# Optimization experiments

Hardware: AMD Instinct MI355X
Metric: run time of the kernel (lower is better)

## Reference

```python
import jax, jax.numpy as jnp
import numpy as np

IN_F = 1024
OUT_F = 4096
BATCH = 1024

def setup_inputs() -> dict:
    key = jax.random.key(0)
    k1, k2, k3, k4 = jax.random.split(key, 4)
    s = np.sqrt(IN_F).astype(np.float32)  # weight init range, as in reset_parameters
    x = jax.random.normal(k1, (BATCH, IN_F), dtype=jnp.float32)
    weights = jax.random.uniform(k2, (OUT_F, IN_F), minval=-s, maxval=s, dtype=jnp.float32)
    centers = 0.1 * jax.random.normal(k3, (OUT_F, IN_F), dtype=jnp.float32)
    # sigmas ~ U(in-0.5, in+0.5); inv_covar = 1/sigmas
    sigmas = jax.random.uniform(k4, (OUT_F, IN_F), minval=IN_F - 0.5, maxval=IN_F + 0.5, dtype=jnp.float32)
    inv_covar = 1.0 / sigmas
    return {"x": x, "weights": weights, "centers": centers, "inv_covar": inv_covar}

def reference(x, weights, centers, inv_covar):
    # linear part with FGN bias: b_i = -sum_j W_ij * C_ij
    biases = -jnp.sum(weights * centers, axis=-1)  # (O,)
    l = x @ weights.T + biases                      # (B, O)
    # diag Mahalanobis: g_bi = sum_j (x_bj - c_ij)^2 * ic_ij^2
    # expanded to GEMMs to avoid the (B, O, I) broadcast intermediate
    ic2 = inv_covar * inv_covar                     # (O, I)
    g = ((x * x) @ ic2.T
         - 2.0 * (x @ (centers * ic2).T)
         + jnp.sum(centers * centers * ic2, axis=-1))  # (B, O)
    return l * jnp.exp(-g)
```

## Files before the change

### kernel.cpp

```cpp
#include <hip/hip_runtime.h>
#include <hip/hip_bf16.h>
#include <stdint.h>


typedef __attribute__((ext_vector_type(8))) __bf16 bf16x8;
typedef __attribute__((ext_vector_type(16))) float f32x16;

#define G_SCALE 8388608.0f
#define G_INV   1.1920929e-7f

__device__ __forceinline__ unsigned short f2bf(float f) {
  union { float f; unsigned int u; } v; v.f = f;
  unsigned int u = v.u;
  return (unsigned short)((u + 0x7FFFu + ((u >> 16) & 1u)) >> 16);
}

__device__ __forceinline__ unsigned int f2f8(float f) {
  union { float f; unsigned int u; } v; v.f = f;
  unsigned int u = v.u;
  unsigned int s = (u >> 31) << 7;
  unsigned int e = (u >> 23) & 255u;
  if (e < 121u) return s;
  unsigned int q = ((e - 120u) << 23) | (u & 0x7FFFFFu);
  unsigned int r = (q + 0x7FFFFu + ((q >> 20) & 1u)) >> 20;
  if (r > 126u) r = 126u;
  return s | r;
}

__device__ __forceinline__ unsigned long long pack8f8(const float* x) {
  unsigned long long r = 0;
#pragma unroll
  for (int j = 0; j < 8; ++j) r |= (unsigned long long)f2f8(x[j]) << (8 * j);
  return r;
}

__global__ __launch_bounds__(256) void prep(
    const float* __restrict__ X, const float* __restrict__ W,
    const float* __restrict__ C, const float* __restrict__ IC,
    unsigned short* __restrict__ Wb, char* __restrict__ GBb,
    unsigned short* __restrict__ Xb, char* __restrict__ XQb,
    float* __restrict__ bias, float* __restrict__ dvec) {
  const int b = blockIdx.x;
  const int lane = threadIdx.x & 63;
  if (b < 1024) {
    const int row = b * 4 + (threadIdx.x >> 6);
    const float4* W4 = (const float4*)W + (size_t)row * 256 + lane * 4;
    const float4* C4 = (const float4*)C + (size_t)row * 256 + lane * 4;
    const float4* I4 = (const float4*)IC + (size_t)row * 256 + lane * 4;
    float wv[16], cv[16], i2[16], m2[16], i2s[16];
    float swc = 0.f, sd = 0.f;
#pragma unroll
    for (int p = 0; p < 4; ++p) {
      float4 w = W4[p], c = C4[p], ic = I4[p];
      wv[4*p] = w.x; wv[4*p+1] = w.y; wv[4*p+2] = w.z; wv[4*p+3] = w.w;
      cv[4*p] = c.x; cv[4*p+1] = c.y; cv[4*p+2] = c.z; cv[4*p+3] = c.w;
      i2[4*p] = ic.x*ic.x; i2[4*p+1] = ic.y*ic.y; i2[4*p+2] = ic.z*ic.z; i2[4*p+3] = ic.w*ic.w;
    }
#pragma unroll
    for (int j = 0; j < 16; ++j) {
      swc += wv[j] * cv[j];
      sd  += cv[j] * cv[j] * i2[j];
      i2s[j] = i2[j] * G_SCALE;
      m2[j]  = -2.f * cv[j] * i2[j] * G_SCALE;
    }
    ushort4* Wo = (ushort4*)Wb + (size_t)row * 256 + lane * 4;
#pragma unroll
    for (int p = 0; p < 4; ++p) {
      ushort4 a;
      a.x = f2bf(wv[4*p]); a.y = f2bf(wv[4*p+1]);
      a.z = f2bf(wv[4*p+2]); a.w = f2bf(wv[4*p+3]);
      Wo[p] = a;
    }
    ulonglong2* gb = (ulonglong2*)(GBb + (size_t)row * 2048 + lane * 32);
    ulonglong2 u0, u1;
    u0.x = pack8f8(i2s);     u0.y = pack8f8(m2);
    u1.x = pack8f8(i2s + 8); u1.y = pack8f8(m2 + 8);
    gb[0] = u0; gb[1] = u1;
#pragma unroll
    for (int off = 32; off > 0; off >>= 1) {
      swc += __shfl_down(swc, off);
      sd  += __shfl_down(sd, off);
    }
    if (lane == 0) { bias[row] = -swc; dvec[row] = sd; }
  } else {
    const int row = (b - 1024) * 4 + (threadIdx.x >> 6);
    const float4* X4 = (const float4*)X + (size_t)row * 256 + lane * 4;
    float xv[16], qv[16];
#pragma unroll
    for (int p = 0; p < 4; ++p) {
      float4 x = X4[p];
      xv[4*p] = x.x; xv[4*p+1] = x.y; xv[4*p+2] = x.z; xv[4*p+3] = x.w;
    }
#pragma unroll
    for (int j = 0; j < 16; ++j) qv[j] = xv[j] * xv[j];
    ushort4* Xo = (ushort4*)Xb + (size_t)row * 256 + lane * 4;
#pragma unroll
    for (int p = 0; p < 4; ++p) {
      ushort4 a;
      a.x = f2bf(xv[4*p]); a.y = f2bf(xv[4*p+1]);
      a.z = f2bf(xv[4*p+2]); a.w = f2bf(xv[4*p+3]);
      Xo[p] = a;
    }
    ulonglong2* xq = (ulonglong2*)(XQb + (size_t)row * 2048 + lane * 32);
    ulonglong2 u0, u1;
    u0.x = pack8f8(qv);     u0.y = pack8f8(xv);
    u1.x = pack8f8(qv + 8); u1.y = pack8f8(xv + 8);
    xq[0] = u0; xq[1] = u1;
  }
}

#define GLD16(gp, lp)                                                          \
  __builtin_amdgcn_global_load_lds(                                            \
      (const __attribute__((address_space(1))) unsigned int*)(gp),             \
      (__attribute__((address_space(3))) unsigned int*)(lp), 16, 0, 0)

__global__ __launch_bounds__(256, 2) void fgn_gemm(
    const char* __restrict__ Xb, const char* __restrict__ XQb,
    const char* __restrict__ Wb, const char* __restrict__ GBb,
    const float* __restrict__ bias, const float* __restrict__ dvec,
    float* __restrict__ out) {
  __shared__ char smem[73728];
  const int t = threadIdx.x;
  const int m0 = blockIdx.y * 128;
  const int n0 = blockIdx.x * 64;

  const int srow = t >> 2;
  const int gof = ((t & 3) ^ ((srow >> 1) & 3)) * 16;
  const char* gX  = Xb  + (size_t)(m0 + srow) * 2048 + gof;
  const char* gXQ = XQb + (size_t)(m0 + srow) * 2048 + gof;
  const char* gW  = Wb  + (size_t)(n0 + srow) * 2048 + gof;
  const char* gGB = GBb + (size_t)(n0 + srow) * 2048 + gof;

#define LBASE(B) (smem + (size_t)(B) * 24576)
#define STAGE(B, S)                                                            \
  do {                                                                         \
    const int ko = (S) * 64;                                                   \
    char* lb = LBASE(B);                                                       \
    GLD16(gX + ko,           lb + t * 16);                                     \
    GLD16(gX + ko + 131072,  lb + 4096 + t * 16);                              \
    GLD16(gXQ + ko,          lb + 8192 + t * 16);                              \
    GLD16(gXQ + ko + 131072, lb + 12288 + t * 16);                             \
    GLD16(gW + ko,           lb + 16384 + t * 16);                             \
    GLD16(gGB + ko,          lb + 20480 + t * 16);                             \
  } while (0)

  const int wave = t >> 6, lane = t & 63;
  const int wy = wave >> 1, wx = wave & 1;
  const int ln = lane & 31, kh = lane >> 5;
  const int sw = (ln >> 1) & 3;

  int arow[2];
#pragma unroll
  for (int mt = 0; mt < 2; ++mt) arow[mt] = (wy * 64 + mt * 32 + ln) * 64;
  const int brow = (wx * 32 + ln) * 64;

  f32x16 accL[2], accG[2];
#pragma unroll
  for (int mt = 0; mt < 2; ++mt) { accL[mt] = (f32x16)0.f; accG[mt] = (f32x16)0.f; }

#define COMPUTE(B)                                                             \
  do {                                                                         \
    char* lb = LBASE(B);                                                       \
    _Pragma("unroll")                                                          \
    for (int ks = 0; ks < 2; ++ks) {                                           \
      const int u16 = ((2 * ks + kh) ^ sw) * 16;                               \
      bf16x8 ax0 = *(const bf16x8*)(lb + arow[0] + u16);                       \
      bf16x8 ax1 = *(const bf16x8*)(lb + arow[1] + u16);                       \
      long2 xq0 = *(const long2*)(lb + 8192 + arow[0] + u16);                  \
      long2 xq1 = *(const long2*)(lb + 8192 + arow[1] + u16);                  \
      bf16x8 bw = *(const bf16x8*)(lb + 16384 + brow + u16);                   \
      long2 gb  = *(const long2*)(lb + 20480 + brow + u16);                    \
      accL[0] = __builtin_amdgcn_mfma_f32_32x32x16_bf16(ax0, bw, accL[0], 0, 0, 0); \
      accL[1] = __builtin_amdgcn_mfma_f32_32x32x16_bf16(ax1, bw, accL[1], 0, 0, 0); \
      accG[0] = __builtin_amdgcn_mfma_f32_32x32x16_fp8_fp8(xq0.x, gb.x, accG[0], 0, 0, 0); \
      accG[1] = __builtin_amdgcn_mfma_f32_32x32x16_fp8_fp8(xq1.x, gb.x, accG[1], 0, 0, 0); \
      accG[0] = __builtin_amdgcn_mfma_f32_32x32x16_fp8_fp8(xq0.y, gb.y, accG[0], 0, 0, 0); \
      accG[1] = __builtin_amdgcn_mfma_f32_32x32x16_fp8_fp8(xq1.y, gb.y, accG[1], 0, 0, 0); \
    }                                                                          \
  } while (0)

  STAGE(0, 0);
  STAGE(1, 1);
#pragma unroll 1
  for (int s = 0; s < 31; ++s) {
    __builtin_amdgcn_s_waitcnt(0x0076);
    __builtin_amdgcn_s_barrier();
    COMPUTE(s % 3);
    if (s < 30) STAGE((s + 2) % 3, s + 2);
  }
  __builtin_amdgcn_s_waitcnt(0x0070);
  __builtin_amdgcn_s_barrier();
  COMPUTE(31 % 3);

  const int col = n0 + wx * 32 + ln;
  const float bn = bias[col], dn = dvec[col];
#pragma unroll
  for (int mt = 0; mt < 2; ++mt) {
    const int rb = m0 + wy * 64 + mt * 32 + 4 * kh;
#pragma unroll
    for (int r = 0; r < 16; ++r) {
      const int row = rb + (r & 3) + 8 * (r >> 2);
      const float l = accL[mt][r] + bn;
      const float g = accG[mt][r] * G_INV + dn;
      out[(size_t)row * 4096 + col] = l * __expf(-g);
    }
  }
#undef STAGE
#undef COMPUTE
#undef LBASE
}

extern "C" void kernel_launch(void* const* d_in, const int* in_sizes, int n_in,
                              void* d_out, int out_size, void* d_ws, size_t ws_size,
                              hipStream_t stream) {
  const float* x  = (const float*)d_in[0];
  const float* W  = (const float*)d_in[1];
  const float* C  = (const float*)d_in[2];
  const float* IC = (const float*)d_in[3];
  float* out = (float*)d_out;

  char* ws = (char*)d_ws;
  unsigned short* Wb  = (unsigned short*)(ws);
  char*           GBb = ws + (8u << 20);
  unsigned short* Xb  = (unsigned short*)(ws + (16u << 20));
  char*           XQb = ws + (18u << 20);
  float* bias = (float*)(ws + (20u << 20));
  float* dvec = (float*)(ws + (20u << 20) + 16384);

  hipLaunchKernelGGL(prep, dim3(1280), dim3(256), 0, stream, x, W, C, IC,
                     Wb, GBb, Xb, XQb, bias, dvec);
  hipLaunchKernelGGL(fgn_gemm, dim3(64, 8), dim3(256), 0, stream,
                     Xb ? (const char*)Xb : nullptr, XQb,
                     (const char*)Wb, GBb, bias, dvec, out);
}
```

Before: 128.5 us.

## Pre-swizzle operands into MFMA fragment layout and load directly to registers with split-K waves

The prep kernel now writes X, X², W and the Gaussian operands in a fragment-major layout, so each lane's MFMA operand is one contiguous 16-byte load. The GEMM drops LDS staging and barriers in the main loop and software-pipelines global loads straight into registers. It uses 512-thread blocks split into two K halves, each wave computing a 64x64 tile, with partial sums reduced through shared memory before the epilogue. This removes LDS traffic and per-stage barriers, at the cost of relying on L2/global latency hiding with only one-deep register prefetch and adding a reduction step.

After: 147.4 us. 14.6% more time.

```diff
diff --git a/kernel.cpp b/kernel.cpp
--- a/kernel.cpp
+++ b/kernel.cpp
@@ -4,15 +4,25 @@
 
 
 typedef __attribute__((ext_vector_type(8))) __bf16 bf16x8;
+typedef __attribute__((ext_vector_type(4))) float f32x4;
 typedef __attribute__((ext_vector_type(16))) float f32x16;
 
 #define G_SCALE 8388608.0f
 #define G_INV   1.1920929e-7f
 
-__device__ __forceinline__ unsigned short f2bf(float f) {
+__device__ __forceinline__ unsigned int f2bf(float f) {
   union { float f; unsigned int u; } v; v.f = f;
   unsigned int u = v.u;
-  return (unsigned short)((u + 0x7FFFu + ((u >> 16) & 1u)) >> 16);
+  return (u + 0x7FFFu + ((u >> 16) & 1u)) >> 16;
+}
+
+__device__ __forceinline__ uint4 pack8bf(const float* v) {
+  uint4 r;
+  r.x = f2bf(v[0]) | (f2bf(v[1]) << 16);
+  r.y = f2bf(v[2]) | (f2bf(v[3]) << 16);
+  r.z = f2bf(v[4]) | (f2bf(v[5]) << 16);
+  r.w = f2bf(v[6]) | (f2bf(v[7]) << 16);
+  return r;
 }
 
 __device__ __forceinline__ unsigned int f2f8(float f) {
@@ -37,8 +47,8 @@
 __global__ __launch_bounds__(256) void prep(
     const float* __restrict__ X, const float* __restrict__ W,
     const float* __restrict__ C, const float* __restrict__ IC,
-    unsigned short* __restrict__ Wb, char* __restrict__ GBb,
-    unsigned short* __restrict__ Xb, char* __restrict__ XQb,
+    uint4* __restrict__ Wf, ulonglong2* __restrict__ GBf,
+    uint4* __restrict__ Xf, ulonglong2* __restrict__ XQf,
     float* __restrict__ bias, float* __restrict__ dvec) {
   const int b = blockIdx.x;
   const int lane = threadIdx.x & 63;
@@ -47,14 +57,15 @@
     const float4* W4 = (const float4*)W + (size_t)row * 256 + lane * 4;
     const float4* C4 = (const float4*)C + (size_t)row * 256 + lane * 4;
     const float4* I4 = (const float4*)IC + (size_t)row * 256 + lane * 4;
-    float wv[16], cv[16], i2[16], m2[16], i2s[16];
+    float wv[16], cv[16], i2[16], i2s[16], m2[16];
     float swc = 0.f, sd = 0.f;
 #pragma unroll
     for (int p = 0; p < 4; ++p) {
       float4 w = W4[p], c = C4[p], ic = I4[p];
       wv[4*p] = w.x; wv[4*p+1] = w.y; wv[4*p+2] = w.z; wv[4*p+3] = w.w;
       cv[4*p] = c.x; cv[4*p+1] = c.y; cv[4*p+2] = c.z; cv[4*p+3] = c.w;
-      i2[4*p] = ic.x*ic.x; i2[4*p+1] = ic.y*ic.y; i2[4*p+2] = ic.z*ic.z; i2[4*p+3] = ic.w*ic.w;
+      i2[4*p] = ic.x*ic.x; i2[4*p+1] = ic.y*ic.y;
+      i2[4*p+2] = ic.z*ic.z; i2[4*p+3] = ic.w*ic.w;
     }
 #pragma unroll
     for (int j = 0; j < 16; ++j) {
@@ -63,19 +74,13 @@
       i2s[j] = i2[j] * G_SCALE;
       m2[j]  = -2.f * cv[j] * i2[j] * G_SCALE;
     }
-    ushort4* Wo = (ushort4*)Wb + (size_t)row * 256 + lane * 4;
-#pragma unroll
-    for (int p = 0; p < 4; ++p) {
-      ushort4 a;
-      a.x = f2bf(wv[4*p]); a.y = f2bf(wv[4*p+1]);
-      a.z = f2bf(wv[4*p+2]); a.w = f2bf(wv[4*p+3]);
-      Wo[p] = a;
-    }
-    ulonglong2* gb = (ulonglong2*)(GBb + (size_t)row * 2048 + lane * 32);
-    ulonglong2 u0, u1;
-    u0.x = pack8f8(i2s);     u0.y = pack8f8(m2);
-    u1.x = pack8f8(i2s + 8); u1.y = pack8f8(m2 + 8);
-    gb[0] = u0; gb[1] = u1;
+    const size_t idx = ((size_t)(row >> 5) * 64 + lane) * 64 + (row & 31);
+    Wf[idx]      = pack8bf(wv);
+    Wf[idx + 32] = pack8bf(wv + 8);
+    ulonglong2 g0, g1;
+    g0.x = pack8f8(i2s);     g0.y = pack8f8(m2);
+    g1.x = pack8f8(i2s + 8); g1.y = pack8f8(m2 + 8);
+    GBf[idx] = g0; GBf[idx + 32] = g1;
 #pragma unroll
     for (int off = 32; off > 0; off >>= 1) {
       swc += __shfl_down(swc, off);
@@ -93,121 +98,159 @@
     }
 #pragma unroll
     for (int j = 0; j < 16; ++j) qv[j] = xv[j] * xv[j];
-    ushort4* Xo = (ushort4*)Xb + (size_t)row * 256 + lane * 4;
-#pragma unroll
-    for (int p = 0; p < 4; ++p) {
-      ushort4 a;
-      a.x = f2bf(xv[4*p]); a.y = f2bf(xv[4*p+1]);
-      a.z = f2bf(xv[4*p+2]); a.w = f2bf(xv[4*p+3]);
-      Xo[p] = a;
-    }
-    ulonglong2* xq = (ulonglong2*)(XQb + (size_t)row * 2048 + lane * 32);
-    ulonglong2 u0, u1;
-    u0.x = pack8f8(qv);     u0.y = pack8f8(xv);
-    u1.x = pack8f8(qv + 8); u1.y = pack8f8(xv + 8);
-    xq[0] = u0; xq[1] = u1;
-  }
-}
-
-#define GLD16(gp, lp)                                                          \
-  __builtin_amdgcn_global_load_lds(                                            \
-      (const __attribute__((address_space(1))) unsigned int*)(gp),             \
-      (__attribute__((address_space(3))) unsigned int*)(lp), 16, 0, 0)
-
-__global__ __launch_bounds__(256, 2) void fgn_gemm(
-    const char* __restrict__ Xb, const char* __restrict__ XQb,
-    const char* __restrict__ Wb, const char* __restrict__ GBb,
+    const size_t idx = ((size_t)(row >> 5) * 64 + lane) * 64 + (row & 31);
+    Xf[idx]      = pack8bf(xv);
+    Xf[idx + 32] = pack8bf(xv + 8);
+    ulonglong2 q0, q1;
+    q0.x = pack8f8(qv);     q0.y = pack8f8(xv);
+    q1.x = pack8f8(qv + 8); q1.y = pack8f8(xv + 8);
+    XQf[idx] = q0; XQf[idx + 32] = q1;
+  }
+}
+
+__global__ __launch_bounds__(512, 2) void fgn_gemm(
+    const uint4* __restrict__ Xf, const uint4* __restrict__ XQf,
+    const uint4* __restrict__ Wf, const uint4* __restrict__ GBf,
     const float* __restrict__ bias, const float* __restrict__ dvec,
     float* __restrict__ out) {
-  __shared__ char smem[73728];
+  __shared__ float red[16384];
   const int t = threadIdx.x;
-  const int m0 = blockIdx.y * 128;
-  const int n0 = blockIdx.x * 64;
-
-  const int srow = t >> 2;
-  const int gof = ((t & 3) ^ ((srow >> 1) & 3)) * 16;
-  const char* gX  = Xb  + (size_t)(m0 + srow) * 2048 + gof;
-  const char* gXQ = XQb + (size_t)(m0 + srow) * 2048 + gof;
-  const char* gW  = Wb  + (size_t)(n0 + srow) * 2048 + gof;
-  const char* gGB = GBb + (size_t)(n0 + srow) * 2048 + gof;
-
-#define LBASE(B) (smem + (size_t)(B) * 24576)
-#define STAGE(B, S)                                                            \
+  const int wave = t >> 6, lane = t & 63;
+  const int kg = wave >> 2, wy = (wave >> 1) & 1, wx = wave & 1;
+  const int mb0 = blockIdx.y * 4 + wy * 2;
+  const int nb0 = blockIdx.x * 4 + wx * 2;
+
+  const uint4 *pa[2], *pq[2], *pw[2], *pg[2];
+#pragma unroll
+  for (int i = 0; i < 2; ++i) {
+    const size_t ai = ((size_t)(mb0 + i) * 64 + kg * 32) * 64 + lane;
+    const size_t bi = ((size_t)(nb0 + i) * 64 + kg * 32) * 64 + lane;
+    pa[i] = Xf + ai;  pq[i] = XQf + ai;
+    pw[i] = Wf + bi;  pg[i] = GBf + bi;
+  }
+
+  f32x16 accL[2][2], accG[2][2];
+#pragma unroll
+  for (int i = 0; i < 2; ++i)
+#pragma unroll
+    for (int j = 0; j < 2; ++j) { accL[i][j] = (f32x16)0.f; accG[i][j] = (f32x16)0.f; }
+
+  uint4 ax0[2], xq0[2], bw0[2], gb0[2];
+#pragma unroll
+  for (int i = 0; i < 2; ++i) {
+    ax0[i] = pa[i][0]; xq0[i] = pq[i][0];
+    bw0[i] = pw[i][0]; gb0[i] = pg[i][0];
+    pa[i] += 64; pq[i] += 64; pw[i] += 64; pg[i] += 64;
+  }
+
+#define COMPUTE(AX, XQ, BW, GB)                                                \
   do {                                                                         \
-    const int ko = (S) * 64;                                                   \
-    char* lb = LBASE(B);                                                       \
-    GLD16(gX + ko,           lb + t * 16);                                     \
-    GLD16(gX + ko + 131072,  lb + 4096 + t * 16);                              \
-    GLD16(gXQ + ko,          lb + 8192 + t * 16);                              \
-    GLD16(gXQ + ko + 131072, lb + 12288 + t * 16);                             \
-    GLD16(gW + ko,           lb + 16384 + t * 16);                             \
-    GLD16(gGB + ko,          lb + 20480 + t * 16);                             \
-  } while (0)
-
-  const int wave = t >> 6, lane = t & 63;
-  const int wy = wave >> 1, wx = wave & 1;
-  const int ln = lane & 31, kh = lane >> 5;
-  const int sw = (ln >> 1) & 3;
-
-  int arow[2];
-#pragma unroll
-  for (int mt = 0; mt < 2; ++mt) arow[mt] = (wy * 64 + mt * 32 + ln) * 64;
-  const int brow = (wx * 32 + ln) * 64;
-
-  f32x16 accL[2], accG[2];
-#pragma unroll
-  for (int mt = 0; mt < 2; ++mt) { accL[mt] = (f32x16)0.f; accG[mt] = (f32x16)0.f; }
-
-#define COMPUTE(B)                                                             \
-  do {                                                                         \
-    char* lb = LBASE(B);                                                       \
     _Pragma("unroll")                                                          \
-    for (int ks = 0; ks < 2; ++ks) {                                           \
-      const int u16 = ((2 * ks + kh) ^ sw) * 16;                               \
-      bf16x8 ax0 = *(const bf16x8*)(lb + arow[0] + u16);                       \
-      bf16x8 ax1 = *(const bf16x8*)(lb + arow[1] + u16);                       \
-      long2 xq0 = *(const long2*)(lb + 8192 + arow[0] + u16);                  \
-      long2 xq1 = *(const long2*)(lb + 8192 + arow[1] + u16);                  \
-      bf16x8 bw = *(const bf16x8*)(lb + 16384 + brow + u16);                   \
-      long2 gb  = *(const long2*)(lb + 20480 + brow + u16);                    \
-      accL[0] = __builtin_amdgcn_mfma_f32_32x32x16_bf16(ax0, bw, accL[0], 0, 0, 0); \
-      accL[1] = __builtin_amdgcn_mfma_f32_32x32x16_bf16(ax1, bw, accL[1], 0, 0, 0); \
-      accG[0] = __builtin_amdgcn_mfma_f32_32x32x16_fp8_fp8(xq0.x, gb.x, accG[0], 0, 0, 0); \
-      accG[1] = __builtin_amdgcn_mfma_f32_32x32x16_fp8_fp8(xq1.x, gb.x, accG[1], 0, 0, 0); \
-      accG[0] = __builtin_amdgcn_mfma_f32_32x32x16_fp8_fp8(xq0.y, gb.y, accG[0], 0, 0, 0); \
-      accG[1] = __builtin_amdgcn_mfma_f32_32x32x16_fp8_fp8(xq1.y, gb.y, accG[1], 0, 0, 0); \
+    for (int i = 0; i < 2; ++i) {                                              \
+      bf16x8 a = __builtin_bit_cast(bf16x8, (AX)[i]);                          \
+      long2 q  = __builtin_bit_cast(long2, (XQ)[i]);                           \
+      _Pragma("unroll")                                                        \
+      for (int j = 0; j < 2; ++j) {                                            \
+        bf16x8 w = __builtin_bit_cast(bf16x8, (BW)[j]);                        \
+        long2 g  = __builtin_bit_cast(long2, (GB)[j]);                         \
+        accL[i][j] = __builtin_amdgcn_mfma_f32_32x32x16_bf16(a, w, accL[i][j], 0, 0, 0); \
+        accG[i][j] = __builtin_amdgcn_mfma_f32_32x32x16_fp8_fp8(q.x, g.x, accG[i][j], 0, 0, 0); \
+        accG[i][j] = __builtin_amdgcn_mfma_f32_32x32x16_fp8_fp8(q.y, g.y, accG[i][j], 0, 0, 0); \
+      }                                                                        \
     }                                                                          \
   } while (0)
 
-  STAGE(0, 0);
-  STAGE(1, 1);
-#pragma unroll 1
+#pragma unroll
   for (int s = 0; s < 31; ++s) {
-    __builtin_amdgcn_s_waitcnt(0x0076);
-    __builtin_amdgcn_s_barrier();
-    COMPUTE(s % 3);
-    if (s < 30) STAGE((s + 2) % 3, s + 2);
-  }
-  __builtin_amdgcn_s_waitcnt(0x0070);
-  __builtin_amdgcn_s_barrier();
-  COMPUTE(31 % 3);
-
-  const int col = n0 + wx * 32 + ln;
-  const float bn = bias[col], dn = dvec[col];
-#pragma unroll
-  for (int mt = 0; mt < 2; ++mt) {
-    const int rb = m0 + wy * 64 + mt * 32 + 4 * kh;
-#pragma unroll
-    for (int r = 0; r < 16; ++r) {
-      const int row = rb + (r & 3) + 8 * (r >> 2);
-      const float l = accL[mt][r] + bn;
-      const float g = accG[mt][r] * G_INV + dn;
-      out[(size_t)row * 4096 + col] = l * __expf(-g);
-    }
-  }
-#undef STAGE
+    uint4 ax1[2], xq1[2], bw1[2], gb1[2];
+#pragma unroll
+    for (int i = 0; i < 2; ++i) {
+      ax1[i] = pa[i][0]; xq1[i] = pq[i][0];
+      bw1[i] = pw[i][0]; gb1[i] = pg[i][0];
+      pa[i] += 64; pq[i] += 64; pw[i] += 64; pg[i] += 64;
+    }
+    COMPUTE(ax0, xq0, bw0, gb0);
+#pragma unroll
+    for (int i = 0; i < 2; ++i) {
+      ax0[i] = ax1[i]; xq0[i] = xq1[i]; bw0[i] = bw1[i]; gb0[i] = gb1[i];
+    }
+  }
+  COMPUTE(ax0, xq0, bw0, gb0);
+
+  f32x4* slot = (f32x4*)(red + (size_t)(wy * 2 + wx) * 4096);
+  if (kg == 1) {
+#pragma unroll
+    for (int i = 0; i < 2; ++i)
+#pragma unroll
+      for (int j = 0; j < 2; ++j) {
+        const int fr = i * 2 + j;
+#pragma unroll
+        for (int r = 0; r < 4; ++r) {
+          f32x4 c = { accL[i][j][4*r], accL[i][j][4*r+1],
+                      accL[i][j][4*r+2], accL[i][j][4*r+3] };
+          slot[fr * 256 + r * 64 + lane] = c;
+        }
+      }
+  }
+  __syncthreads();
+  if (kg == 0) {
+#pragma unroll
+    for (int i = 0; i < 2; ++i)
+#pragma unroll
+      for (int j = 0; j < 2; ++j) {
+        const int fr = i * 2 + j;
+#pragma unroll
+        for (int r = 0; r < 4; ++r) {
+          f32x4 c = slot[fr * 256 + r * 64 + lane];
+          accL[i][j][4*r]   += c[0]; accL[i][j][4*r+1] += c[1];
+          accL[i][j][4*r+2] += c[2]; accL[i][j][4*r+3] += c[3];
+        }
+      }
+  }
+  __syncthreads();
+  if (kg == 1) {
+#pragma unroll
+    for (int i = 0; i < 2; ++i)
+#pragma unroll
+      for (int j = 0; j < 2; ++j) {
+        const int fr = i * 2 + j;
+#pragma unroll
+        for (int r = 0; r < 4; ++r) {
+          f32x4 c = { accG[i][j][4*r], accG[i][j][4*r+1],
+                      accG[i][j][4*r+2], accG[i][j][4*r+3] };
+          slot[fr * 256 + r * 64 + lane] = c;
+        }
+      }
+  }
+  __syncthreads();
+  if (kg == 0) {
+    const int ln = lane & 31, kh = lane >> 5;
+#pragma unroll
+    for (int j = 0; j < 2; ++j) {
+      const int col = (nb0 + j) * 32 + ln;
+      const float bn = bias[col], dn = dvec[col];
+#pragma unroll
+      for (int i = 0; i < 2; ++i) {
+        const int fr = i * 2 + j;
+        f32x16 gacc = accG[i][j];
+#pragma unroll
+        for (int r = 0; r < 4; ++r) {
+          f32x4 c = slot[fr * 256 + r * 64 + lane];
+          gacc[4*r]   += c[0]; gacc[4*r+1] += c[1];
+          gacc[4*r+2] += c[2]; gacc[4*r+3] += c[3];
+        }
+        const int rb = (mb0 + i) * 32 + 4 * kh;
+#pragma unroll
+        for (int r = 0; r < 16; ++r) {
+          const int row = rb + (r & 3) + 8 * (r >> 2);
+          const float l = accL[i][j][r] + bn;
+          const float g = gacc[r] * G_INV + dn;
+          out[(size_t)row * 4096 + col] = l * __expf(-g);
+        }
+      }
+    }
+  }
 #undef COMPUTE
-#undef LBASE
 }
 
 extern "C" void kernel_launch(void* const* d_in, const int* in_sizes, int n_in,
@@ -220,16 +263,16 @@
   float* out = (float*)d_out;
 
   char* ws = (char*)d_ws;
-  unsigned short* Wb  = (unsigned short*)(ws);
-  char*           GBb = ws + (8u << 20);
-  unsigned short* Xb  = (unsigned short*)(ws + (16u << 20));
-  char*           XQb = ws + (18u << 20);
+  uint4*      Wf  = (uint4*)(ws);
+  ulonglong2* GBf = (ulonglong2*)(ws + (8u << 20));
+  uint4*      Xf  = (uint4*)(ws + (16u << 20));
+  ulonglong2* XQf = (ulonglong2*)(ws + (18u << 20));
   float* bias = (float*)(ws + (20u << 20));
   float* dvec = (float*)(ws + (20u << 20) + 16384);
 
   hipLaunchKernelGGL(prep, dim3(1280), dim3(256), 0, stream, x, W, C, IC,
-                     Wb, GBb, Xb, XQb, bias, dvec);
-  hipLaunchKernelGGL(fgn_gemm, dim3(64, 8), dim3(256), 0, stream,
-                     Xb ? (const char*)Xb : nullptr, XQb,
-                     (const char*)Wb, GBb, bias, dvec, out);
-}
+                     Wf, GBf, Xf, XQf, bias, dvec);
+  hipLaunchKernelGGL(fgn_gemm, dim3(32, 8), dim3(512), 0, stream,
+                     Xf, (const uint4*)XQf, Wf, (const uint4*)GBf,
+                     bias, dvec, out);
+}
```
